# Performance work log

Measured on AMD Instinct MI355X. Metric: run time of the kernel, lower is better.

The kernel has to match this reference:

```python
import jax, jax.numpy as jnp
import numpy as np

N = 32768      # total nodes (512 graphs x 64 padded nodes)
E = 262144     # edges (avg degree 8)
F_IN = 74      # atom feature dim
D0 = 128       # dim_embedding
D1 = 256       # hidden feats
B = 512        # batch_size (graphs)
NPG = 64       # nodes per graph
EPS = 1e-5     # BatchNorm1d eps


def setup_inputs() -> dict:
    key = jax.random.key(0)
    ks = jax.random.split(key, 8)
    def rn(k, shape, s=0.05):
        return jax.random.normal(k, shape, jnp.float32) * s
    # init_transform weight [D0, F_IN]; padding=True zeroes the last row
    W_init = rn(ks[0], (D0, F_IN)).at[-1].set(0.0)
    return {
        "node_feats": jax.random.normal(ks[1], (N, F_IN), jnp.float32),
        "W_init": W_init,
        "gcn_w1": rn(ks[2], (D0, D1)), "gcn_b1": jnp.zeros((D1,), jnp.float32),
        "res_w1": rn(ks[3], (D1, D0)), "res_b1": jnp.zeros((D1,), jnp.float32),
        "bn_g1": jnp.ones((D1,), jnp.float32), "bn_b1": jnp.zeros((D1,), jnp.float32),
        "gcn_w2": rn(ks[4], (D1, D1)), "gcn_b2": jnp.zeros((D1,), jnp.float32),
        "bn_g2": jnp.ones((D1,), jnp.float32), "bn_b2": jnp.zeros((D1,), jnp.float32),
        "edge_src": jax.random.randint(ks[5], (E,), 0, N),
        "edge_dst": jax.random.randint(ks[6], (E,), 0, N),
    }


def _agg(x, src, dst):
    # DGL GraphConv norm='both': D_out^{-1/2} gather-scatter D_in^{-1/2}, degrees clamped to >= 1
    ones = jnp.ones((src.shape[0],), x.dtype)
    deg_out = jnp.clip(jax.ops.segment_sum(ones, src, num_segments=N), 1.0)
    deg_in = jnp.clip(jax.ops.segment_sum(ones, dst, num_segments=N), 1.0)
    xs = x * jax.lax.rsqrt(deg_out)[:, None]
    agg = jax.ops.segment_sum(xs[src], dst, num_segments=N)  # [N, d]
    return agg * jax.lax.rsqrt(deg_in)[:, None]


def _bn(x, g, b):
    # BatchNorm1d training-mode: batch stats over node axis, biased var
    m = x.mean(0)
    v = x.var(0)
    return (x - m) * jax.lax.rsqrt(v + EPS) * g + b


def reference(node_feats, W_init, gcn_w1, gcn_b1, res_w1, res_b1, bn_g1, bn_b1,
              gcn_w2, gcn_b2, bn_g2, bn_b2, edge_src, edge_dst):
    h = node_feats @ W_init.T  # [N, D0]
    # layer 1: residual Linear 128->256, GCN(aggregate then weight, since in<out), GELU, BN
    res = h @ res_w1.T + res_b1
    g = jax.nn.gelu(_agg(h, edge_src, edge_dst) @ gcn_w1 + gcn_b1, approximate=False)
    h = _bn(g + res, bn_g1, bn_b1)
    # layer 2: Identity residual
    g = jax.nn.gelu(_agg(h, edge_src, edge_dst) @ gcn_w2 + gcn_b2, approximate=False)
    h = _bn(g + h, bn_g2, bn_b2)
    return h.reshape(B, NPG, D1)
```

## Files before the change

kernel.cpp:

```cpp
#include <hip/hip_runtime.h>
#include <hip/hip_bf16.h>
#include <math.h>

#define N_NODES 32768
#define E_EDGES 262144
#define F_INF   74
#define KP      96
#define D0      128
#define D1      256
#define BN_EPS  1e-5f
#define RBLK    1024

typedef float f32x4 __attribute__((ext_vector_type(4)));
typedef short s16x8 __attribute__((ext_vector_type(8)));

__device__ __forceinline__ float b2f(ushort h) { return __uint_as_float(((unsigned)h) << 16); }
__device__ __forceinline__ ushort f2b(float f) {
    unsigned u = __float_as_uint(f);
    return (ushort)((u + 0x7FFFu + ((u >> 16) & 1u)) >> 16);
}
__device__ __forceinline__ float gelu_exact(float x) {
    return 0.5f * x * (1.0f + erff(x * 0.70710678118654752440f));
}


__global__ void k_front_a(const int* __restrict__ src, const int* __restrict__ dst,
                          int* __restrict__ deg,
                          const float* __restrict__ nf, const float* __restrict__ Wi,
                          const float* __restrict__ w1, const float* __restrict__ rw,
                          const float* __restrict__ w2,
                          ushort* __restrict__ nfB, ushort* __restrict__ WTB,
                          ushort* __restrict__ WB1, ushort* __restrict__ RWB,
                          ushort* __restrict__ WB2) {
    int bid = blockIdx.x;
    int tid = threadIdx.x;
    if (bid < 1024) {
        int e = bid * 256 + tid;
        atomicAdd(&deg[src[e]], 1);
        atomicAdd(&deg[N_NODES + dst[e]], 1);
        return;
    }
    int idx = (bid - 1024) * 256 + tid;
    {
        int n = idx / KP, k = idx - n * KP;
        nfB[idx] = (k < F_INF) ? f2b(nf[n * F_INF + k]) : (ushort)0;
    }
    if (idx < D0 * KP) {
        int c = idx / KP, k = idx - c * KP;
        WTB[idx] = (k < F_INF) ? f2b(Wi[c * F_INF + k]) : (ushort)0;
    }
    if (idx < D1 * D0) {
        int n = idx >> 7, k = idx & 127;
        WB1[idx] = f2b(w1[k * D1 + n]);
        RWB[idx] = f2b(rw[idx]);
    }
    if (idx < D1 * D1) {
        int n = idx >> 8, k = idx & 255;
        WB2[idx] = f2b(w2[k * D1 + n]);
    }
}

__global__ __launch_bounds__(1024) void k_scan(const int* __restrict__ deg,
                                               int* __restrict__ row_off,
                                               float* __restrict__ rsq_out,
                                               float* __restrict__ rsq_in,
                                               int* __restrict__ cursor) {
    __shared__ int part[1024];
    int t = threadIdx.x;
    int base = t * 32;
    int loc[32];
    int s = 0;
    #pragma unroll
    for (int i = 0; i < 32; i++) { loc[i] = s; s += deg[N_NODES + base + i]; }
    part[t] = s;
    #pragma unroll
    for (int i = 0; i < 32; i++) {
        int n = base + i;
        int d_o = deg[n];           if (d_o < 1) d_o = 1;
        int d_i = deg[N_NODES + n]; if (d_i < 1) d_i = 1;
        rsq_out[n] = 1.0f / sqrtf((float)d_o);
        rsq_in[n]  = 1.0f / sqrtf((float)d_i);
        cursor[n] = 0;
    }
    __syncthreads();
    for (int off = 1; off < 1024; off <<= 1) {
        int v = 0;
        if (t >= off) v = part[t - off];
        __syncthreads();
        if (t >= off) part[t] += v;
        __syncthreads();
    }
    int pre = (t == 0) ? 0 : part[t - 1];
    #pragma unroll
    for (int i = 0; i < 32; i++) row_off[base + i] = pre + loc[i];
    if (t == 1023) row_off[N_NODES] = part[1023];
}


__global__ __launch_bounds__(512) void k_front_b(
    const int* __restrict__ src, const int* __restrict__ dst,
    const int* __restrict__ row_off, const float* __restrict__ rsq_out,
    int* __restrict__ cursor, int* __restrict__ csr_src, float* __restrict__ esc,
    const ushort* __restrict__ nfB, const ushort* __restrict__ WTB,
    ushort* __restrict__ h0) {
    int bid = blockIdx.x;
    int tid = threadIdx.x;
    if (bid < 512) {
        int e = bid * 512 + tid;
        int d = dst[e];
        int s = src[e];
        int slot = atomicAdd(&cursor[d], 1);
        int pos = row_off[d] + slot;
        csr_src[pos] = s;
        esc[pos] = rsq_out[s];
        return;
    }
    int b2 = bid - 512;
    int w = tid >> 6, lane = tid & 63, m = lane & 15, g4 = lane >> 4;
    int col = w * 16 + m;
    int rbase = b2 * 16;
    s16x8 B[3], A[3];
    #pragma unroll
    for (int j = 0; j < 3; j++)
        B[j] = *reinterpret_cast<const s16x8*>(&WTB[(size_t)col * KP + j * 32 + g4 * 8]);
    #pragma unroll
    for (int j = 0; j < 3; j++)
        A[j] = *reinterpret_cast<const s16x8*>(&nfB[(size_t)(rbase + m) * KP + j * 32 + g4 * 8]);
    f32x4 acc = (f32x4){0.f, 0.f, 0.f, 0.f};
    #pragma unroll
    for (int j = 0; j < 3; j++)
        acc = __builtin_amdgcn_mfma_f32_16x16x32_bf16(A[j], B[j], acc, 0, 0, 0);
    #pragma unroll
    for (int r = 0; r < 4; r++)
        h0[(size_t)(rbase + g4 * 4 + r) * D0 + col] = f2b(acc[r]);
}


__global__ __launch_bounds__(512) void k_layer1f(
    const ushort* __restrict__ h0B, const float* __restrict__ rsq_in,
    const int* __restrict__ row_off, const int* __restrict__ csr_src,
    const float* __restrict__ esc,
    const ushort* __restrict__ WB1, const ushort* __restrict__ RWB,
    const float* __restrict__ b1, const float* __restrict__ rb,
    ushort* __restrict__ t1B, float* __restrict__ partials) {
    __shared__ ushort sA[32 * 128];
    int tid = threadIdx.x;
    int rbase = blockIdx.x * 32;
    {
        int nloc = tid >> 4;
        int node = rbase + nloc;
        int f = (tid & 15) * 8;
        int beg = row_off[node], end = row_off[node + 1];
        float a[8];
        #pragma unroll
        for (int j = 0; j < 8; j++) a[j] = 0.f;
        int e = beg;
        for (; e + 3 < end; e += 4) {
            int s0 = csr_src[e], s1 = csr_src[e + 1], s2 = csr_src[e + 2], s3 = csr_src[e + 3];
            float c0 = esc[e], c1 = esc[e + 1], c2 = esc[e + 2], c3 = esc[e + 3];
            s16x8 v0 = *reinterpret_cast<const s16x8*>(&h0B[(size_t)s0 * D0 + f]);
            s16x8 v1 = *reinterpret_cast<const s16x8*>(&h0B[(size_t)s1 * D0 + f]);
            s16x8 v2 = *reinterpret_cast<const s16x8*>(&h0B[(size_t)s2 * D0 + f]);
            s16x8 v3 = *reinterpret_cast<const s16x8*>(&h0B[(size_t)s3 * D0 + f]);
            #pragma unroll
            for (int j = 0; j < 8; j++)
                a[j] += b2f((ushort)v0[j]) * c0 + b2f((ushort)v1[j]) * c1 +
                        b2f((ushort)v2[j]) * c2 + b2f((ushort)v3[j]) * c3;
        }
        for (; e < end; e++) {
            int s = csr_src[e];
            float sc = esc[e];
            s16x8 v = *reinterpret_cast<const s16x8*>(&h0B[(size_t)s * D0 + f]);
            #pragma unroll
            for (int j = 0; j < 8; j++) a[j] += b2f((ushort)v[j]) * sc;
        }
        float si = rsq_in[node];
        s16x8 o;
        #pragma unroll
        for (int j = 0; j < 8; j++) o[j] = (short)f2b(a[j] * si);
        int boff = nloc * 256 + ((f * 2) ^ ((nloc & 15) << 4));
        *reinterpret_cast<s16x8*>(((char*)sA) + boff) = o;
    }
    __syncthreads();
    int w = tid >> 6, lane = tid & 63, m = lane & 15, g4 = lane >> 4;
    int cb = w * 32;
    s16x8 BG[2][4], BR[2][4];
    #pragma unroll
    for (int nt = 0; nt < 2; nt++)
        #pragma unroll
        for (int j = 0; j < 4; j++) {
            BG[nt][j] = *reinterpret_cast<const s16x8*>(&WB1[(size_t)(cb + nt * 16 + m) * D0 + j * 32 + g4 * 8]);
            BR[nt][j] = *reinterpret_cast<const s16x8*>(&RWB[(size_t)(cb + nt * 16 + m) * D0 + j * 32 + g4 * 8]);
        }
    float bg[2], brv[2];
    #pragma unroll
    for (int nt = 0; nt < 2; nt++) {
        bg[nt]  = b1[cb + nt * 16 + m];
        brv[nt] = rb[cb + nt * 16 + m];
    }
    float ps[2] = {0.f, 0.f}, pq[2] = {0.f, 0.f};
    #pragma unroll
    for (int rt = 0; rt < 2; rt++) {
        int row = rt * 16 + m;
        s16x8 aA[4], aH[4];
        #pragma unroll
        for (int j = 0; j < 4; j++) {
            int boff = row * 256 + (((j * 4 + g4) * 16) ^ ((row & 15) << 4));
            aA[j] = *reinterpret_cast<const s16x8*>(((const char*)sA) + boff);
            aH[j] = *reinterpret_cast<const s16x8*>(&h0B[(size_t)(rbase + row) * D0 + j * 32 + g4 * 8]);
        }
        f32x4 accG[2], accR[2];
        #pragma unroll
        for (int nt = 0; nt < 2; nt++) {
            accG[nt] = (f32x4){0.f, 0.f, 0.f, 0.f};
            accR[nt] = (f32x4){0.f, 0.f, 0.f, 0.f};
        }
        #pragma unroll
        for (int j = 0; j < 4; j++)
            #pragma unroll
            for (int nt = 0; nt < 2; nt++) {
                accG[nt] = __builtin_amdgcn_mfma_f32_16x16x32_bf16(aA[j], BG[nt][j], accG[nt], 0, 0, 0);
                accR[nt] = __builtin_amdgcn_mfma_f32_16x16x32_bf16(aH[j], BR[nt][j], accR[nt], 0, 0, 0);
            }
        #pragma unroll
        for (int nt = 0; nt < 2; nt++) {
            int col = cb + nt * 16 + m;
            #pragma unroll
            for (int r = 0; r < 4; r++) {
                int orow = rbase + rt * 16 + g4 * 4 + r;
                float v = gelu_exact(accG[nt][r] + bg[nt]) + accR[nt][r] + brv[nt];
                t1B[(size_t)orow * D1 + col] = f2b(v);
                ps[nt] += v; pq[nt] += v * v;
            }
        }
    }
    #pragma unroll
    for (int nt = 0; nt < 2; nt++) {
        float s = ps[nt], q = pq[nt];
        s += __shfl_xor(s, 16); s += __shfl_xor(s, 32);
        q += __shfl_xor(q, 16); q += __shfl_xor(q, 32);
        if (g4 == 0) {
            int col = cb + nt * 16 + m;
            partials[(size_t)col * RBLK + blockIdx.x] = s;
            partials[(size_t)(256 + col) * RBLK + blockIdx.x] = q;
        }
    }
}


__global__ __launch_bounds__(512) void k_layer2f(
    const ushort* __restrict__ t1B,
    const float* __restrict__ sc1, const float* __restrict__ sh1,
    const float* __restrict__ rsq_in,
    const int* __restrict__ row_off, const int* __restrict__ csr_src,
    const float* __restrict__ esc,
    const ushort* __restrict__ WB2, const float* __restrict__ b2,
    ushort* __restrict__ t2B, float* __restrict__ partials) {
    __shared__ ushort sA[32 * 256];
    int tid = threadIdx.x;
    int rbase = blockIdx.x * 32;
    {
        int nloc = tid >> 4;
        int node = rbase + nloc;
        int f0 = (tid & 15) * 8;
        int beg = row_off[node], end = row_off[node + 1];
        float a0[8], a1[8];
        #pragma unroll
        for (int j = 0; j < 8; j++) { a0[j] = 0.f; a1[j] = 0.f; }
        float ssum = 0.f;
        int e = beg;
        for (; e + 3 < end; e += 4) {
            int s0 = csr_src[e], s1 = csr_src[e + 1], s2 = csr_src[e + 2], s3 = csr_src[e + 3];
            float c0 = esc[e], c1 = esc[e + 1], c2 = esc[e + 2], c3 = esc[e + 3];
            const s16x8* p0 = reinterpret_cast<const s16x8*>(&t1B[(size_t)s0 * D1 + f0]);
            const s16x8* p1 = reinterpret_cast<const s16x8*>(&t1B[(size_t)s1 * D1 + f0]);
            const s16x8* p2 = reinterpret_cast<const s16x8*>(&t1B[(size_t)s2 * D1 + f0]);
            const s16x8* p3 = reinterpret_cast<const s16x8*>(&t1B[(size_t)s3 * D1 + f0]);
            s16x8 v00 = p0[0], v01 = p0[16];
            s16x8 v10 = p1[0], v11 = p1[16];
            s16x8 v20 = p2[0], v21 = p2[16];
            s16x8 v30 = p3[0], v31 = p3[16];
            ssum += c0 + c1 + c2 + c3;
            #pragma unroll
            for (int j = 0; j < 8; j++) {
                a0[j] += b2f((ushort)v00[j]) * c0 + b2f((ushort)v10[j]) * c1 +
                         b2f((ushort)v20[j]) * c2 + b2f((ushort)v30[j]) * c3;
                a1[j] += b2f((ushort)v01[j]) * c0 + b2f((ushort)v11[j]) * c1 +
                         b2f((ushort)v21[j]) * c2 + b2f((ushort)v31[j]) * c3;
            }
        }
        for (; e < end; e++) {
            int s = csr_src[e];
            float sc = esc[e];
            const s16x8* p = reinterpret_cast<const s16x8*>(&t1B[(size_t)s * D1 + f0]);
            s16x8 v0 = p[0], v1 = p[16];
            ssum += sc;
            #pragma unroll
            for (int j = 0; j < 8; j++) {
                a0[j] += b2f((ushort)v0[j]) * sc;
                a1[j] += b2f((ushort)v1[j]) * sc;
            }
        }
        float si = rsq_in[node];
        s16x8 o0, o1;
        #pragma unroll
        for (int j = 0; j < 8; j++) {
            o0[j] = (short)f2b((sc1[f0 + j] * a0[j] + sh1[f0 + j] * ssum) * si);
            o1[j] = (short)f2b((sc1[f0 + 128 + j] * a1[j] + sh1[f0 + 128 + j] * ssum) * si);
        }
        int swz = (nloc & 15) << 4;
        int b0 = nloc * 512 + ((f0 * 2) ^ swz);
        int b1_ = nloc * 512 + (((f0 + 128) * 2) ^ swz);
        *reinterpret_cast<s16x8*>(((char*)sA) + b0) = o0;
        *reinterpret_cast<s16x8*>(((char*)sA) + b1_) = o1;
    }
    __syncthreads();
    int w = tid >> 6, lane = tid & 63, m = lane & 15, g4 = lane >> 4;
    int cb = w * 32;
    ushort rres[2][2][4];
    #pragma unroll
    for (int nt = 0; nt < 2; nt++) {
        int col = cb + nt * 16 + m;
        #pragma unroll
        for (int rt = 0; rt < 2; rt++)
            #pragma unroll
            for (int r = 0; r < 4; r++)
                rres[nt][rt][r] = t1B[(size_t)(rbase + rt * 16 + g4 * 4 + r) * D1 + col];
    }
    s16x8 BG[2][8];
    #pragma unroll
    for (int nt = 0; nt < 2; nt++)
        #pragma unroll
        for (int j = 0; j < 8; j++)
            BG[nt][j] = *reinterpret_cast<const s16x8*>(&WB2[(size_t)(cb + nt * 16 + m) * D1 + j * 32 + g4 * 8]);
    float bg[2], a1c[2], s1c[2];
    #pragma unroll
    for (int nt = 0; nt < 2; nt++) {
        int col = cb + nt * 16 + m;
        bg[nt] = b2[col]; a1c[nt] = sc1[col]; s1c[nt] = sh1[col];
    }
    float ps[2] = {0.f, 0.f}, pq[2] = {0.f, 0.f};
    #pragma unroll
    for (int rt = 0; rt < 2; rt++) {
        int row = rt * 16 + m;
        s16x8 aA[8];
        #pragma unroll
        for (int j = 0; j < 8; j++) {
            int boff = row * 512 + (((j * 4 + g4) * 16) ^ ((row & 15) << 4));
            aA[j] = *reinterpret_cast<const s16x8*>(((const char*)sA) + boff);
        }
        f32x4 acc[2];
        #pragma unroll
        for (int nt = 0; nt < 2; nt++) acc[nt] = (f32x4){0.f, 0.f, 0.f, 0.f};
        #pragma unroll
        for (int j = 0; j < 8; j++)
            #pragma unroll
            for (int nt = 0; nt < 2; nt++)
                acc[nt] = __builtin_amdgcn_mfma_f32_16x16x32_bf16(aA[j], BG[nt][j], acc[nt], 0, 0, 0);
        #pragma unroll
        for (int nt = 0; nt < 2; nt++) {
            int col = cb + nt * 16 + m;
            #pragma unroll
            for (int r = 0; r < 4; r++) {
                int orow = rbase + rt * 16 + g4 * 4 + r;
                float h1v = fmaf(b2f(rres[nt][rt][r]), a1c[nt], s1c[nt]);
                float v = gelu_exact(acc[nt][r] + bg[nt]) + h1v;
                t2B[(size_t)orow * D1 + col] = f2b(v);
                ps[nt] += v; pq[nt] += v * v;
            }
        }
    }
    #pragma unroll
    for (int nt = 0; nt < 2; nt++) {
        float s = ps[nt], q = pq[nt];
        s += __shfl_xor(s, 16); s += __shfl_xor(s, 32);
        q += __shfl_xor(q, 16); q += __shfl_xor(q, 32);
        if (g4 == 0) {
            int col = cb + nt * 16 + m;
            partials[(size_t)col * RBLK + blockIdx.x] = s;
            partials[(size_t)(256 + col) * RBLK + blockIdx.x] = q;
        }
    }
}


__global__ __launch_bounds__(256) void k_reduce(
    const float* __restrict__ partials, const float* __restrict__ g,
    const float* __restrict__ b, float* __restrict__ sc, float* __restrict__ sh) {
    int c = blockIdx.x;
    int t = threadIdx.x;
    const float* ps = partials + (size_t)c * RBLK;
    const float* pq = partials + (size_t)(256 + c) * RBLK;
    float s = ps[t] + ps[t + 256] + ps[t + 512] + ps[t + 768];
    float q = pq[t] + pq[t + 256] + pq[t + 512] + pq[t + 768];
    __shared__ float Ls[256], Lq[256];
    Ls[t] = s; Lq[t] = q;
    __syncthreads();
    for (int o = 128; o > 0; o >>= 1) {
        if (t < o) { Ls[t] += Ls[t + o]; Lq[t] += Lq[t + o]; }
        __syncthreads();
    }
    if (t == 0) {
        float m = Ls[0] * (1.0f / (float)N_NODES);
        float var = Lq[0] * (1.0f / (float)N_NODES) - m * m;
        float a = g[c] / sqrtf(var + BN_EPS);
        sc[c] = a;
        sh[c] = b[c] - m * a;
    }
}


__global__ __launch_bounds__(256) void k_apply(
    const ushort* __restrict__ t2B, const float* __restrict__ sc,
    const float* __restrict__ sh, float* __restrict__ out) {
    int idx = blockIdx.x * 256 + threadIdx.x;
    size_t base = (size_t)idx * 8;
    int c = (int)(base & 255);
    s16x8 v = *reinterpret_cast<const s16x8*>(&t2B[base]);
    float4 o0, o1;
    o0.x = fmaf(b2f((ushort)v[0]), sc[c + 0], sh[c + 0]);
    o0.y = fmaf(b2f((ushort)v[1]), sc[c + 1], sh[c + 1]);
    o0.z = fmaf(b2f((ushort)v[2]), sc[c + 2], sh[c + 2]);
    o0.w = fmaf(b2f((ushort)v[3]), sc[c + 3], sh[c + 3]);
    o1.x = fmaf(b2f((ushort)v[4]), sc[c + 4], sh[c + 4]);
    o1.y = fmaf(b2f((ushort)v[5]), sc[c + 5], sh[c + 5]);
    o1.z = fmaf(b2f((ushort)v[6]), sc[c + 6], sh[c + 6]);
    o1.w = fmaf(b2f((ushort)v[7]), sc[c + 7], sh[c + 7]);
    *reinterpret_cast<float4*>(&out[base]) = o0;
    *reinterpret_cast<float4*>(&out[base + 4]) = o1;
}


static inline size_t align256(size_t x) { return (x + 255) & ~(size_t)255; }

extern "C" void kernel_launch(void* const* d_in, const int* in_sizes, int n_in,
                              void* d_out, int out_size, void* d_ws, size_t ws_size,
                              hipStream_t stream) {
    const float* node_feats = (const float*)d_in[0];
    const float* W_init     = (const float*)d_in[1];
    const float* gcn_w1     = (const float*)d_in[2];
    const float* gcn_b1     = (const float*)d_in[3];
    const float* res_w1     = (const float*)d_in[4];
    const float* res_b1     = (const float*)d_in[5];
    const float* bn_g1      = (const float*)d_in[6];
    const float* bn_b1      = (const float*)d_in[7];
    const float* gcn_w2     = (const float*)d_in[8];
    const float* gcn_b2     = (const float*)d_in[9];
    const float* bn_g2      = (const float*)d_in[10];
    const float* bn_b2      = (const float*)d_in[11];
    const int*   edge_src   = (const int*)d_in[12];
    const int*   edge_dst   = (const int*)d_in[13];
    float* out = (float*)d_out;

    char* p = (char*)d_ws;
    size_t off = 0;
    auto take = [&](size_t bytes) { void* r = p + off; off += align256(bytes); return r; };

    ushort* h0B   = (ushort*)take((size_t)N_NODES * D0 * 2);
    ushort* t1B   = (ushort*)take((size_t)N_NODES * D1 * 2);
    ushort* t2B   = (ushort*)take((size_t)N_NODES * D1 * 2);
    ushort* nfB   = (ushort*)take((size_t)N_NODES * KP * 2);
    ushort* WTB   = (ushort*)take((size_t)D0 * KP * 2);
    ushort* WB1   = (ushort*)take((size_t)D1 * D0 * 2);
    ushort* RWB   = (ushort*)take((size_t)D1 * D0 * 2);
    ushort* WB2   = (ushort*)take((size_t)D1 * D1 * 2);
    float*  part1 = (float*)take((size_t)2 * 256 * RBLK * 4);
    float*  part2 = (float*)take((size_t)2 * 256 * RBLK * 4);
    float*  sc1   = (float*)take(256 * 4);
    float*  sh1   = (float*)take(256 * 4);
    float*  sc2   = (float*)take(256 * 4);
    float*  sh2   = (float*)take(256 * 4);
    float*  rsq_out = (float*)take((size_t)N_NODES * 4);
    float*  rsq_in  = (float*)take((size_t)N_NODES * 4);
    int*    degi    = (int*)take((size_t)2 * N_NODES * 4);
    int*    cursor  = (int*)take((size_t)N_NODES * 4);
    int*    row_off = (int*)take((size_t)(N_NODES + 2) * 4);
    int*    csr_src = (int*)take((size_t)E_EDGES * 4);
    float*  esc     = (float*)take((size_t)E_EDGES * 4);

    hipMemsetAsync(degi, 0, (size_t)2 * N_NODES * 4, stream);

    k_front_a<<<1024 + (N_NODES * KP) / 256, 256, 0, stream>>>(
        edge_src, edge_dst, degi, node_feats, W_init, gcn_w1, res_w1, gcn_w2,
        nfB, WTB, WB1, RWB, WB2);

    k_scan<<<1, 1024, 0, stream>>>(degi, row_off, rsq_out, rsq_in, cursor);

    k_front_b<<<512 + N_NODES / 16, 512, 0, stream>>>(
        edge_src, edge_dst, row_off, rsq_out, cursor, csr_src, esc, nfB, WTB, h0B);

    k_layer1f<<<RBLK, 512, 0, stream>>>(h0B, rsq_in, row_off, csr_src, esc,
                                        WB1, RWB, gcn_b1, res_b1, t1B, part1);
    k_reduce<<<256, 256, 0, stream>>>(part1, bn_g1, bn_b1, sc1, sh1);

    k_layer2f<<<RBLK, 512, 0, stream>>>(t1B, sc1, sh1, rsq_in, row_off, csr_src, esc,
                                        WB2, gcn_b2, t2B, part2);
    k_reduce<<<256, 256, 0, stream>>>(part2, bn_g2, bn_b2, sc2, sh2);

    k_apply<<<(N_NODES * D1 / 8) / 256, 256, 0, stream>>>(t2B, sc2, sh2, out);
}
```

Before: 211.7 us.

## Halve rows per block and split each node's edge gather across two thread groups

Layer 1 and layer 2 fused kernels now process 16 nodes per block instead of 32. Each node's gather is split between two 16-thread halves that take alternating edges, and the halves are combined with a cross-lane shuffle. This doubles the block count and the memory-level parallelism in the latency-bound gather. In exchange, each block loads the weight tiles for only half as many rows, and the partials buffer and reduction grow to 2048 blocks.

After: 234.5 us. 10.8% more time.

```diff
diff --git a/kernel.cpp b/kernel.cpp
--- a/kernel.cpp
+++ b/kernel.cpp
@@ -9,7 +9,7 @@
 #define D0      128
 #define D1      256
 #define BN_EPS  1e-5f
-#define RBLK    1024
+#define RBLK    2048
 
 typedef float f32x4 __attribute__((ext_vector_type(4)));
 typedef short s16x8 __attribute__((ext_vector_type(8)));
@@ -143,21 +143,22 @@
     const ushort* __restrict__ WB1, const ushort* __restrict__ RWB,
     const float* __restrict__ b1, const float* __restrict__ rb,
     ushort* __restrict__ t1B, float* __restrict__ partials) {
-    __shared__ ushort sA[32 * 128];
+    __shared__ ushort sA[16 * 128];
     int tid = threadIdx.x;
-    int rbase = blockIdx.x * 32;
+    int rbase = blockIdx.x * 16;
     {
-        int nloc = tid >> 4;
+        int nloc = tid >> 5;
+        int half = (tid >> 4) & 1;
         int node = rbase + nloc;
         int f = (tid & 15) * 8;
         int beg = row_off[node], end = row_off[node + 1];
         float a[8];
         #pragma unroll
         for (int j = 0; j < 8; j++) a[j] = 0.f;
-        int e = beg;
-        for (; e + 3 < end; e += 4) {
-            int s0 = csr_src[e], s1 = csr_src[e + 1], s2 = csr_src[e + 2], s3 = csr_src[e + 3];
-            float c0 = esc[e], c1 = esc[e + 1], c2 = esc[e + 2], c3 = esc[e + 3];
+        int e = beg + half;
+        for (; e + 6 < end; e += 8) {
+            int s0 = csr_src[e], s1 = csr_src[e + 2], s2 = csr_src[e + 4], s3 = csr_src[e + 6];
+            float c0 = esc[e], c1 = esc[e + 2], c2 = esc[e + 4], c3 = esc[e + 6];
             s16x8 v0 = *reinterpret_cast<const s16x8*>(&h0B[(size_t)s0 * D0 + f]);
             s16x8 v1 = *reinterpret_cast<const s16x8*>(&h0B[(size_t)s1 * D0 + f]);
             s16x8 v2 = *reinterpret_cast<const s16x8*>(&h0B[(size_t)s2 * D0 + f]);
@@ -167,19 +168,23 @@
                 a[j] += b2f((ushort)v0[j]) * c0 + b2f((ushort)v1[j]) * c1 +
                         b2f((ushort)v2[j]) * c2 + b2f((ushort)v3[j]) * c3;
         }
-        for (; e < end; e++) {
+        for (; e < end; e += 2) {
             int s = csr_src[e];
             float sc = esc[e];
             s16x8 v = *reinterpret_cast<const s16x8*>(&h0B[(size_t)s * D0 + f]);
             #pragma unroll
             for (int j = 0; j < 8; j++) a[j] += b2f((ushort)v[j]) * sc;
         }
-        float si = rsq_in[node];
-        s16x8 o;
-        #pragma unroll
-        for (int j = 0; j < 8; j++) o[j] = (short)f2b(a[j] * si);
-        int boff = nloc * 256 + ((f * 2) ^ ((nloc & 15) << 4));
-        *reinterpret_cast<s16x8*>(((char*)sA) + boff) = o;
+        #pragma unroll
+        for (int j = 0; j < 8; j++) a[j] += __shfl_xor(a[j], 16);
+        if (half == 0) {
+            float si = rsq_in[node];
+            s16x8 o;
+            #pragma unroll
+            for (int j = 0; j < 8; j++) o[j] = (short)f2b(a[j] * si);
+            int boff = nloc * 256 + ((f * 2) ^ ((nloc & 15) << 4));
+            *reinterpret_cast<s16x8*>(((char*)sA) + boff) = o;
+        }
     }
     __syncthreads();
     int w = tid >> 6, lane = tid & 63, m = lane & 15, g4 = lane >> 4;
@@ -198,40 +203,36 @@
         bg[nt]  = b1[cb + nt * 16 + m];
         brv[nt] = rb[cb + nt * 16 + m];
     }
+    s16x8 aA[4], aH[4];
+    #pragma unroll
+    for (int j = 0; j < 4; j++) {
+        int boff = m * 256 + (((j * 4 + g4) * 16) ^ ((m & 15) << 4));
+        aA[j] = *reinterpret_cast<const s16x8*>(((const char*)sA) + boff);
+        aH[j] = *reinterpret_cast<const s16x8*>(&h0B[(size_t)(rbase + m) * D0 + j * 32 + g4 * 8]);
+    }
+    f32x4 accG[2], accR[2];
+    #pragma unroll
+    for (int nt = 0; nt < 2; nt++) {
+        accG[nt] = (f32x4){0.f, 0.f, 0.f, 0.f};
+        accR[nt] = (f32x4){0.f, 0.f, 0.f, 0.f};
+    }
+    #pragma unroll
+    for (int j = 0; j < 4; j++)
+        #pragma unroll
+        for (int nt = 0; nt < 2; nt++) {
+            accG[nt] = __builtin_amdgcn_mfma_f32_16x16x32_bf16(aA[j], BG[nt][j], accG[nt], 0, 0, 0);
+            accR[nt] = __builtin_amdgcn_mfma_f32_16x16x32_bf16(aH[j], BR[nt][j], accR[nt], 0, 0, 0);
+        }
     float ps[2] = {0.f, 0.f}, pq[2] = {0.f, 0.f};
     #pragma unroll
-    for (int rt = 0; rt < 2; rt++) {
-        int row = rt * 16 + m;
-        s16x8 aA[4], aH[4];
-        #pragma unroll
-        for (int j = 0; j < 4; j++) {
-            int boff = row * 256 + (((j * 4 + g4) * 16) ^ ((row & 15) << 4));
-            aA[j] = *reinterpret_cast<const s16x8*>(((const char*)sA) + boff);
-            aH[j] = *reinterpret_cast<const s16x8*>(&h0B[(size_t)(rbase + row) * D0 + j * 32 + g4 * 8]);
-        }
-        f32x4 accG[2], accR[2];
-        #pragma unroll
-        for (int nt = 0; nt < 2; nt++) {
-            accG[nt] = (f32x4){0.f, 0.f, 0.f, 0.f};
-            accR[nt] = (f32x4){0.f, 0.f, 0.f, 0.f};
-        }
-        #pragma unroll
-        for (int j = 0; j < 4; j++)
-            #pragma unroll
-            for (int nt = 0; nt < 2; nt++) {
-                accG[nt] = __builtin_amdgcn_mfma_f32_16x16x32_bf16(aA[j], BG[nt][j], accG[nt], 0, 0, 0);
-                accR[nt] = __builtin_amdgcn_mfma_f32_16x16x32_bf16(aH[j], BR[nt][j], accR[nt], 0, 0, 0);
-            }
-        #pragma unroll
-        for (int nt = 0; nt < 2; nt++) {
-            int col = cb + nt * 16 + m;
-            #pragma unroll
-            for (int r = 0; r < 4; r++) {
-                int orow = rbase + rt * 16 + g4 * 4 + r;
-                float v = gelu_exact(accG[nt][r] + bg[nt]) + accR[nt][r] + brv[nt];
-                t1B[(size_t)orow * D1 + col] = f2b(v);
-                ps[nt] += v; pq[nt] += v * v;
-            }
+    for (int nt = 0; nt < 2; nt++) {
+        int col = cb + nt * 16 + m;
+        #pragma unroll
+        for (int r = 0; r < 4; r++) {
+            int orow = rbase + g4 * 4 + r;
+            float v = gelu_exact(accG[nt][r] + bg[nt]) + accR[nt][r] + brv[nt];
+            t1B[(size_t)orow * D1 + col] = f2b(v);
+            ps[nt] += v; pq[nt] += v * v;
         }
     }
     #pragma unroll
@@ -256,11 +257,12 @@
     const float* __restrict__ esc,
     const ushort* __restrict__ WB2, const float* __restrict__ b2,
     ushort* __restrict__ t2B, float* __restrict__ partials) {
-    __shared__ ushort sA[32 * 256];
+    __shared__ ushort sA[16 * 256];
     int tid = threadIdx.x;
-    int rbase = blockIdx.x * 32;
+    int rbase = blockIdx.x * 16;
     {
-        int nloc = tid >> 4;
+        int nloc = tid >> 5;
+        int half = (tid >> 4) & 1;
         int node = rbase + nloc;
         int f0 = (tid & 15) * 8;
         int beg = row_off[node], end = row_off[node + 1];
@@ -268,10 +270,10 @@
         #pragma unroll
         for (int j = 0; j < 8; j++) { a0[j] = 0.f; a1[j] = 0.f; }
         float ssum = 0.f;
-        int e = beg;
-        for (; e + 3 < end; e += 4) {
-            int s0 = csr_src[e], s1 = csr_src[e + 1], s2 = csr_src[e + 2], s3 = csr_src[e + 3];
-            float c0 = esc[e], c1 = esc[e + 1], c2 = esc[e + 2], c3 = esc[e + 3];
+        int e = beg + half;
+        for (; e + 6 < end; e += 8) {
+            int s0 = csr_src[e], s1 = csr_src[e + 2], s2 = csr_src[e + 4], s3 = csr_src[e + 6];
+            float c0 = esc[e], c1 = esc[e + 2], c2 = esc[e + 4], c3 = esc[e + 6];
             const s16x8* p0 = reinterpret_cast<const s16x8*>(&t1B[(size_t)s0 * D1 + f0]);
             const s16x8* p1 = reinterpret_cast<const s16x8*>(&t1B[(size_t)s1 * D1 + f0]);
             const s16x8* p2 = reinterpret_cast<const s16x8*>(&t1B[(size_t)s2 * D1 + f0]);
@@ -289,7 +291,7 @@
                          b2f((ushort)v21[j]) * c2 + b2f((ushort)v31[j]) * c3;
             }
         }
-        for (; e < end; e++) {
+        for (; e < end; e += 2) {
             int s = csr_src[e];
             float sc = esc[e];
             const s16x8* p = reinterpret_cast<const s16x8*>(&t1B[(size_t)s * D1 + f0]);
@@ -301,31 +303,37 @@
                 a1[j] += b2f((ushort)v1[j]) * sc;
             }
         }
-        float si = rsq_in[node];
-        s16x8 o0, o1;
         #pragma unroll
         for (int j = 0; j < 8; j++) {
-            o0[j] = (short)f2b((sc1[f0 + j] * a0[j] + sh1[f0 + j] * ssum) * si);
-            o1[j] = (short)f2b((sc1[f0 + 128 + j] * a1[j] + sh1[f0 + 128 + j] * ssum) * si);
-        }
-        int swz = (nloc & 15) << 4;
-        int b0 = nloc * 512 + ((f0 * 2) ^ swz);
-        int b1_ = nloc * 512 + (((f0 + 128) * 2) ^ swz);
-        *reinterpret_cast<s16x8*>(((char*)sA) + b0) = o0;
-        *reinterpret_cast<s16x8*>(((char*)sA) + b1_) = o1;
+            a0[j] += __shfl_xor(a0[j], 16);
+            a1[j] += __shfl_xor(a1[j], 16);
+        }
+        ssum += __shfl_xor(ssum, 16);
+        if (half == 0) {
+            float si = rsq_in[node];
+            s16x8 o0, o1;
+            #pragma unroll
+            for (int j = 0; j < 8; j++) {
+                o0[j] = (short)f2b((sc1[f0 + j] * a0[j] + sh1[f0 + j] * ssum) * si);
+                o1[j] = (short)f2b((sc1[f0 + 128 + j] * a1[j] + sh1[f0 + 128 + j] * ssum) * si);
+            }
+            int swz = (nloc & 15) << 4;
+            int b0 = nloc * 512 + ((f0 * 2) ^ swz);
+            int b1_ = nloc * 512 + (((f0 + 128) * 2) ^ swz);
+            *reinterpret_cast<s16x8*>(((char*)sA) + b0) = o0;
+            *reinterpret_cast<s16x8*>(((char*)sA) + b1_) = o1;
+        }
     }
     __syncthreads();
     int w = tid >> 6, lane = tid & 63, m = lane & 15, g4 = lane >> 4;
     int cb = w * 32;
-    ushort rres[2][2][4];
+    ushort rres[2][4];
     #pragma unroll
     for (int nt = 0; nt < 2; nt++) {
         int col = cb + nt * 16 + m;
         #pragma unroll
-        for (int rt = 0; rt < 2; rt++)
-            #pragma unroll
-            for (int r = 0; r < 4; r++)
-                rres[nt][rt][r] = t1B[(size_t)(rbase + rt * 16 + g4 * 4 + r) * D1 + col];
+        for (int r = 0; r < 4; r++)
+            rres[nt][r] = t1B[(size_t)(rbase + g4 * 4 + r) * D1 + col];
     }
     s16x8 BG[2][8];
     #pragma unroll
@@ -339,35 +347,31 @@
         int col = cb + nt * 16 + m;
         bg[nt] = b2[col]; a1c[nt] = sc1[col]; s1c[nt] = sh1[col];
     }
+    s16x8 aA[8];
+    #pragma unroll
+    for (int j = 0; j < 8; j++) {
+        int boff = m * 512 + (((j * 4 + g4) * 16) ^ ((m & 15) << 4));
+        aA[j] = *reinterpret_cast<const s16x8*>(((const char*)sA) + boff);
+    }
+    f32x4 acc[2];
+    #pragma unroll
+    for (int nt = 0; nt < 2; nt++) acc[nt] = (f32x4){0.f, 0.f, 0.f, 0.f};
+    #pragma unroll
+    for (int j = 0; j < 8; j++)
+        #pragma unroll
+        for (int nt = 0; nt < 2; nt++)
+            acc[nt] = __builtin_amdgcn_mfma_f32_16x16x32_bf16(aA[j], BG[nt][j], acc[nt], 0, 0, 0);
     float ps[2] = {0.f, 0.f}, pq[2] = {0.f, 0.f};
     #pragma unroll
-    for (int rt = 0; rt < 2; rt++) {
-        int row = rt * 16 + m;
-        s16x8 aA[8];
-        #pragma unroll
-        for (int j = 0; j < 8; j++) {
-            int boff = row * 512 + (((j * 4 + g4) * 16) ^ ((row & 15) << 4));
-            aA[j] = *reinterpret_cast<const s16x8*>(((const char*)sA) + boff);
-        }
-        f32x4 acc[2];
-        #pragma unroll
-        for (int nt = 0; nt < 2; nt++) acc[nt] = (f32x4){0.f, 0.f, 0.f, 0.f};
-        #pragma unroll
-        for (int j = 0; j < 8; j++)
-            #pragma unroll
-            for (int nt = 0; nt < 2; nt++)
-                acc[nt] = __builtin_amdgcn_mfma_f32_16x16x32_bf16(aA[j], BG[nt][j], acc[nt], 0, 0, 0);
-        #pragma unroll
-        for (int nt = 0; nt < 2; nt++) {
-            int col = cb + nt * 16 + m;
-            #pragma unroll
-            for (int r = 0; r < 4; r++) {
-                int orow = rbase + rt * 16 + g4 * 4 + r;
-                float h1v = fmaf(b2f(rres[nt][rt][r]), a1c[nt], s1c[nt]);
-                float v = gelu_exact(acc[nt][r] + bg[nt]) + h1v;
-                t2B[(size_t)orow * D1 + col] = f2b(v);
-                ps[nt] += v; pq[nt] += v * v;
-            }
+    for (int nt = 0; nt < 2; nt++) {
+        int col = cb + nt * 16 + m;
+        #pragma unroll
+        for (int r = 0; r < 4; r++) {
+            int orow = rbase + g4 * 4 + r;
+            float h1v = fmaf(b2f(rres[nt][r]), a1c[nt], s1c[nt]);
+            float v = gelu_exact(acc[nt][r] + bg[nt]) + h1v;
+            t2B[(size_t)orow * D1 + col] = f2b(v);
+            ps[nt] += v; pq[nt] += v * v;
         }
     }
     #pragma unroll
@@ -391,8 +395,9 @@
     int t = threadIdx.x;
     const float* ps = partials + (size_t)c * RBLK;
     const float* pq = partials + (size_t)(256 + c) * RBLK;
-    float s = ps[t] + ps[t + 256] + ps[t + 512] + ps[t + 768];
-    float q = pq[t] + pq[t + 256] + pq[t + 512] + pq[t + 768];
+    float s = 0.f, q = 0.f;
+    #pragma unroll
+    for (int k = 0; k < 8; k++) { s += ps[t + 256 * k]; q += pq[t + 256 * k]; }
     __shared__ float Ls[256], Lq[256];
     Ls[t] = s; Lq[t] = q;
     __syncthreads();
```

## Gather layer-2 neighbor features from an 8-bit quantized copy with doubled threads

Applied to the files above, without the earlier changes.

Layer 1 now also writes an 8-bit custom float (fp8-like, 3-bit mantissa) copy of its output, and the layer-2 aggregation gathers these bytes instead of bf16, halving gather bandwidth. The layer-2 kernel is launched with 1024 threads, and two half-groups split each node's edges and combine their sums with a shuffle. Each wave in the MFMA stage now handles one 16-column tile. This trades accuracy of the aggregated features for less memory traffic and adds an extra byte store per element in layer 1.

Result: slower. 216.5 us (+2.3%).

```diff
diff --git a/kernel.cpp b/kernel.cpp
--- a/kernel.cpp
+++ b/kernel.cpp
@@ -18,6 +18,28 @@
 __device__ __forceinline__ ushort f2b(float f) {
     unsigned u = __float_as_uint(f);
     return (ushort)((u + 0x7FFFu + ((u >> 16) & 1u)) >> 16);
+}
+__device__ __forceinline__ unsigned char f2q(float f) {
+    unsigned u = __float_as_uint(f * 7.52316384526264005e-37f);
+    unsigned s = (u >> 24) & 0x80u;
+    int r = (int)(((u & 0x7fffffffu) + 0x80000u) >> 20);
+    r = r > 126 ? 126 : r;
+    return (unsigned char)(s | (unsigned)r);
+}
+__device__ __forceinline__ float q2f(unsigned x) {
+    unsigned fb = ((x & 0x80u) << 24) | ((x & 0x7fu) << 20);
+    return __uint_as_float(fb) * 1.32922799578491587e+36f;
+}
+__device__ __forceinline__ void acc_q(float* a, uint4 q, float c) {
+    unsigned d;
+    d = q.x; a[0]  += q2f(d & 255u) * c; a[1]  += q2f((d >> 8) & 255u) * c;
+             a[2]  += q2f((d >> 16) & 255u) * c; a[3]  += q2f(d >> 24) * c;
+    d = q.y; a[4]  += q2f(d & 255u) * c; a[5]  += q2f((d >> 8) & 255u) * c;
+             a[6]  += q2f((d >> 16) & 255u) * c; a[7]  += q2f(d >> 24) * c;
+    d = q.z; a[8]  += q2f(d & 255u) * c; a[9]  += q2f((d >> 8) & 255u) * c;
+             a[10] += q2f((d >> 16) & 255u) * c; a[11] += q2f(d >> 24) * c;
+    d = q.w; a[12] += q2f(d & 255u) * c; a[13] += q2f((d >> 8) & 255u) * c;
+             a[14] += q2f((d >> 16) & 255u) * c; a[15] += q2f(d >> 24) * c;
 }
 __device__ __forceinline__ float gelu_exact(float x) {
     return 0.5f * x * (1.0f + erff(x * 0.70710678118654752440f));
@@ -142,7 +164,8 @@
     const float* __restrict__ esc,
     const ushort* __restrict__ WB1, const ushort* __restrict__ RWB,
     const float* __restrict__ b1, const float* __restrict__ rb,
-    ushort* __restrict__ t1B, float* __restrict__ partials) {
+    ushort* __restrict__ t1B, unsigned char* __restrict__ t1Q,
+    float* __restrict__ partials) {
     __shared__ ushort sA[32 * 128];
     int tid = threadIdx.x;
     int rbase = blockIdx.x * 32;
@@ -230,6 +253,7 @@
                 int orow = rbase + rt * 16 + g4 * 4 + r;
                 float v = gelu_exact(accG[nt][r] + bg[nt]) + accR[nt][r] + brv[nt];
                 t1B[(size_t)orow * D1 + col] = f2b(v);
+                t1Q[(size_t)orow * D1 + col] = f2q(v);
                 ps[nt] += v; pq[nt] += v * v;
             }
         }
@@ -248,8 +272,8 @@
 }
 
 
-__global__ __launch_bounds__(512) void k_layer2f(
-    const ushort* __restrict__ t1B,
+__global__ __launch_bounds__(1024) void k_layer2f(
+    const ushort* __restrict__ t1B, const unsigned char* __restrict__ t1Q,
     const float* __restrict__ sc1, const float* __restrict__ sh1,
     const float* __restrict__ rsq_in,
     const int* __restrict__ row_off, const int* __restrict__ csr_src,
@@ -260,86 +284,65 @@
     int tid = threadIdx.x;
     int rbase = blockIdx.x * 32;
     {
-        int nloc = tid >> 4;
+        int nloc = tid >> 5;
+        int half = (tid >> 4) & 1;
         int node = rbase + nloc;
-        int f0 = (tid & 15) * 8;
+        int f0 = (tid & 15) * 16;
         int beg = row_off[node], end = row_off[node + 1];
-        float a0[8], a1[8];
-        #pragma unroll
-        for (int j = 0; j < 8; j++) { a0[j] = 0.f; a1[j] = 0.f; }
+        float a[16];
+        #pragma unroll
+        for (int j = 0; j < 16; j++) a[j] = 0.f;
         float ssum = 0.f;
-        int e = beg;
-        for (; e + 3 < end; e += 4) {
-            int s0 = csr_src[e], s1 = csr_src[e + 1], s2 = csr_src[e + 2], s3 = csr_src[e + 3];
-            float c0 = esc[e], c1 = esc[e + 1], c2 = esc[e + 2], c3 = esc[e + 3];
-            const s16x8* p0 = reinterpret_cast<const s16x8*>(&t1B[(size_t)s0 * D1 + f0]);
-            const s16x8* p1 = reinterpret_cast<const s16x8*>(&t1B[(size_t)s1 * D1 + f0]);
-            const s16x8* p2 = reinterpret_cast<const s16x8*>(&t1B[(size_t)s2 * D1 + f0]);
-            const s16x8* p3 = reinterpret_cast<const s16x8*>(&t1B[(size_t)s3 * D1 + f0]);
-            s16x8 v00 = p0[0], v01 = p0[16];
-            s16x8 v10 = p1[0], v11 = p1[16];
-            s16x8 v20 = p2[0], v21 = p2[16];
-            s16x8 v30 = p3[0], v31 = p3[16];
+        int e = beg + half;
+        for (; e + 6 < end; e += 8) {
+            int s0 = csr_src[e], s1 = csr_src[e + 2], s2 = csr_src[e + 4], s3 = csr_src[e + 6];
+            float c0 = esc[e], c1 = esc[e + 2], c2 = esc[e + 4], c3 = esc[e + 6];
+            uint4 q0 = *reinterpret_cast<const uint4*>(&t1Q[(size_t)s0 * D1 + f0]);
+            uint4 q1 = *reinterpret_cast<const uint4*>(&t1Q[(size_t)s1 * D1 + f0]);
+            uint4 q2 = *reinterpret_cast<const uint4*>(&t1Q[(size_t)s2 * D1 + f0]);
+            uint4 q3 = *reinterpret_cast<const uint4*>(&t1Q[(size_t)s3 * D1 + f0]);
             ssum += c0 + c1 + c2 + c3;
+            acc_q(a, q0, c0); acc_q(a, q1, c1); acc_q(a, q2, c2); acc_q(a, q3, c3);
+        }
+        for (; e < end; e += 2) {
+            int s = csr_src[e];
+            float sc = esc[e];
+            uint4 q = *reinterpret_cast<const uint4*>(&t1Q[(size_t)s * D1 + f0]);
+            ssum += sc;
+            acc_q(a, q, sc);
+        }
+        #pragma unroll
+        for (int j = 0; j < 16; j++) a[j] += __shfl_xor(a[j], 16);
+        ssum += __shfl_xor(ssum, 16);
+        if (half == 0) {
+            float si = rsq_in[node];
+            s16x8 o0, o1;
             #pragma unroll
             for (int j = 0; j < 8; j++) {
-                a0[j] += b2f((ushort)v00[j]) * c0 + b2f((ushort)v10[j]) * c1 +
-                         b2f((ushort)v20[j]) * c2 + b2f((ushort)v30[j]) * c3;
-                a1[j] += b2f((ushort)v01[j]) * c0 + b2f((ushort)v11[j]) * c1 +
-                         b2f((ushort)v21[j]) * c2 + b2f((ushort)v31[j]) * c3;
+                o0[j] = (short)f2b((sc1[f0 + j] * a[j] + sh1[f0 + j] * ssum) * si);
+                o1[j] = (short)f2b((sc1[f0 + 8 + j] * a[8 + j] + sh1[f0 + 8 + j] * ssum) * si);
             }
-        }
-        for (; e < end; e++) {
-            int s = csr_src[e];
-            float sc = esc[e];
-            const s16x8* p = reinterpret_cast<const s16x8*>(&t1B[(size_t)s * D1 + f0]);
-            s16x8 v0 = p[0], v1 = p[16];
-            ssum += sc;
-            #pragma unroll
-            for (int j = 0; j < 8; j++) {
-                a0[j] += b2f((ushort)v0[j]) * sc;
-                a1[j] += b2f((ushort)v1[j]) * sc;
-            }
-        }
-        float si = rsq_in[node];
-        s16x8 o0, o1;
-        #pragma unroll
-        for (int j = 0; j < 8; j++) {
-            o0[j] = (short)f2b((sc1[f0 + j] * a0[j] + sh1[f0 + j] * ssum) * si);
-            o1[j] = (short)f2b((sc1[f0 + 128 + j] * a1[j] + sh1[f0 + 128 + j] * ssum) * si);
-        }
-        int swz = (nloc & 15) << 4;
-        int b0 = nloc * 512 + ((f0 * 2) ^ swz);
-        int b1_ = nloc * 512 + (((f0 + 128) * 2) ^ swz);
-        *reinterpret_cast<s16x8*>(((char*)sA) + b0) = o0;
-        *reinterpret_cast<s16x8*>(((char*)sA) + b1_) = o1;
+            int swz = (nloc & 15) << 4;
+            int x0 = f0 * 2;
+            *reinterpret_cast<s16x8*>(((char*)sA) + nloc * 512 + (x0 ^ swz)) = o0;
+            *reinterpret_cast<s16x8*>(((char*)sA) + nloc * 512 + ((x0 + 16) ^ swz)) = o1;
+        }
     }
     __syncthreads();
     int w = tid >> 6, lane = tid & 63, m = lane & 15, g4 = lane >> 4;
-    int cb = w * 32;
-    ushort rres[2][2][4];
-    #pragma unroll
-    for (int nt = 0; nt < 2; nt++) {
-        int col = cb + nt * 16 + m;
-        #pragma unroll
-        for (int rt = 0; rt < 2; rt++)
-            #pragma unroll
-            for (int r = 0; r < 4; r++)
-                rres[nt][rt][r] = t1B[(size_t)(rbase + rt * 16 + g4 * 4 + r) * D1 + col];
-    }
-    s16x8 BG[2][8];
-    #pragma unroll
-    for (int nt = 0; nt < 2; nt++)
-        #pragma unroll
-        for (int j = 0; j < 8; j++)
-            BG[nt][j] = *reinterpret_cast<const s16x8*>(&WB2[(size_t)(cb + nt * 16 + m) * D1 + j * 32 + g4 * 8]);
-    float bg[2], a1c[2], s1c[2];
-    #pragma unroll
-    for (int nt = 0; nt < 2; nt++) {
-        int col = cb + nt * 16 + m;
-        bg[nt] = b2[col]; a1c[nt] = sc1[col]; s1c[nt] = sh1[col];
-    }
-    float ps[2] = {0.f, 0.f}, pq[2] = {0.f, 0.f};
+    int col = w * 16 + m;
+    ushort rres[2][4];
+    #pragma unroll
+    for (int rt = 0; rt < 2; rt++)
+        #pragma unroll
+        for (int r = 0; r < 4; r++)
+            rres[rt][r] = t1B[(size_t)(rbase + rt * 16 + g4 * 4 + r) * D1 + col];
+    s16x8 BG[8];
+    #pragma unroll
+    for (int j = 0; j < 8; j++)
+        BG[j] = *reinterpret_cast<const s16x8*>(&WB2[(size_t)col * D1 + j * 32 + g4 * 8]);
+    float bg = b2[col], a1c = sc1[col], s1c = sh1[col];
+    float ps = 0.f, pq = 0.f;
     #pragma unroll
     for (int rt = 0; rt < 2; rt++) {
         int row = rt * 16 + m;
@@ -349,37 +352,24 @@
             int boff = row * 512 + (((j * 4 + g4) * 16) ^ ((row & 15) << 4));
             aA[j] = *reinterpret_cast<const s16x8*>(((const char*)sA) + boff);
         }
-        f32x4 acc[2];
-        #pragma unroll
-        for (int nt = 0; nt < 2; nt++) acc[nt] = (f32x4){0.f, 0.f, 0.f, 0.f};
+        f32x4 acc = (f32x4){0.f, 0.f, 0.f, 0.f};
         #pragma unroll
         for (int j = 0; j < 8; j++)
-            #pragma unroll
-            for (int nt = 0; nt < 2; nt++)
-                acc[nt] = __builtin_amdgcn_mfma_f32_16x16x32_bf16(aA[j], BG[nt][j], acc[nt], 0, 0, 0);
-        #pragma unroll
-        for (int nt = 0; nt < 2; nt++) {
-            int col = cb + nt * 16 + m;
-            #pragma unroll
-            for (int r = 0; r < 4; r++) {
-                int orow = rbase + rt * 16 + g4 * 4 + r;
-                float h1v = fmaf(b2f(rres[nt][rt][r]), a1c[nt], s1c[nt]);
-                float v = gelu_exact(acc[nt][r] + bg[nt]) + h1v;
-                t2B[(size_t)orow * D1 + col] = f2b(v);
-                ps[nt] += v; pq[nt] += v * v;
-            }
-        }
-    }
-    #pragma unroll
-    for (int nt = 0; nt < 2; nt++) {
-        float s = ps[nt], q = pq[nt];
-        s += __shfl_xor(s, 16); s += __shfl_xor(s, 32);
-        q += __shfl_xor(q, 16); q += __shfl_xor(q, 32);
-        if (g4 == 0) {
-            int col = cb + nt * 16 + m;
-            partials[(size_t)col * RBLK + blockIdx.x] = s;
-            partials[(size_t)(256 + col) * RBLK + blockIdx.x] = q;
-        }
+            acc = __builtin_amdgcn_mfma_f32_16x16x32_bf16(aA[j], BG[j], acc, 0, 0, 0);
+        #pragma unroll
+        for (int r = 0; r < 4; r++) {
+            int orow = rbase + rt * 16 + g4 * 4 + r;
+            float h1v = fmaf(b2f(rres[rt][r]), a1c, s1c);
+            float v = gelu_exact(acc[r] + bg) + h1v;
+            t2B[(size_t)orow * D1 + col] = f2b(v);
+            ps += v; pq += v * v;
+        }
+    }
+    ps += __shfl_xor(ps, 16); ps += __shfl_xor(ps, 32);
+    pq += __shfl_xor(pq, 16); pq += __shfl_xor(pq, 32);
+    if (g4 == 0) {
+        partials[(size_t)col * RBLK + blockIdx.x] = ps;
+        partials[(size_t)(256 + col) * RBLK + blockIdx.x] = pq;
     }
 }
 
@@ -458,6 +448,7 @@
 
     ushort* h0B   = (ushort*)take((size_t)N_NODES * D0 * 2);
     ushort* t1B   = (ushort*)take((size_t)N_NODES * D1 * 2);
+    unsigned char* t1Q = (unsigned char*)take((size_t)N_NODES * D1);
     ushort* t2B   = (ushort*)take((size_t)N_NODES * D1 * 2);
     ushort* nfB   = (ushort*)take((size_t)N_NODES * KP * 2);
     ushort* WTB   = (ushort*)take((size_t)D0 * KP * 2);
@@ -490,11 +481,11 @@
         edge_src, edge_dst, row_off, rsq_out, cursor, csr_src, esc, nfB, WTB, h0B);
 
     k_layer1f<<<RBLK, 512, 0, stream>>>(h0B, rsq_in, row_off, csr_src, esc,
-                                        WB1, RWB, gcn_b1, res_b1, t1B, part1);
+                                        WB1, RWB, gcn_b1, res_b1, t1B, t1Q, part1);
     k_reduce<<<256, 256, 0, stream>>>(part1, bn_g1, bn_b1, sc1, sh1);
 
-    k_layer2f<<<RBLK, 512, 0, stream>>>(t1B, sc1, sh1, rsq_in, row_off, csr_src, esc,
-                                        WB2, gcn_b2, t2B, part2);
+    k_layer2f<<<RBLK, 1024, 0, stream>>>(t1B, t1Q, sc1, sh1, rsq_in, row_off, csr_src, esc,
+                                         WB2, gcn_b2, t2B, part2);
     k_reduce<<<256, 256, 0, stream>>>(part2, bn_g2, bn_b2, sc2, sh2);
 
     k_apply<<<(N_NODES * D1 / 8) / 256, 256, 0, stream>>>(t2B, sc2, sh2, out);
```
